# Kernel optimization log

Hardware: AMD Instinct MI355X
Metric: run time of the kernel (lower is better)

## Reference

```python
import jax, jax.numpy as jnp
import numpy as np

NEG_INF = -1e9
EPS = 1e-9


def setup_inputs() -> dict:
    key = jax.random.key(0)
    ks = jax.random.split(key, 8)
    B, N, H = 128, 256, 512
    s = 1.0 / np.sqrt(H)
    u = lambda k, shape: jax.random.uniform(k, shape, jnp.float32, -s, s)
    return {
        "encoder_outputs": jax.random.normal(ks[0], (B, N, H), jnp.float32),
        "w_ih": u(ks[1], (3 * H, H)),
        "w_hh": u(ks[2], (3 * H, H)),
        "b_ih": u(ks[3], (3 * H,)),
        "b_hh": u(ks[4], (3 * H,)),
        "W1": u(ks[5], (H, H)),
        "W2": u(ks[6], (H, H)),
        "v": u(ks[7], (H,)),
        "decode_steps": 32,
    }


def reference(encoder_outputs, w_ih, w_hh, b_ih, b_hh, W1, W2, v, decode_steps):
    B, N, H = encoder_outputs.shape

    # Loop-invariant: W1 @ encoder_outputs (same math as recomputing per step).
    W1e = jnp.einsum('bnh,kh->bnk', encoder_outputs, W1)  # (B, N, H)

    def gru_cell(x, h):
        gi = x @ w_ih.T + b_ih  # (B, 3H)
        gh = h @ w_hh.T + b_hh  # (B, 3H)
        ir, iz, inn = jnp.split(gi, 3, axis=-1)
        hr, hz, hn = jnp.split(gh, 3, axis=-1)
        r = jax.nn.sigmoid(ir + hr)
        z = jax.nn.sigmoid(iz + hz)
        n = jnp.tanh(inn + r * hn)
        return (1.0 - z) * n + z * h

    def step(carry, _):
        h, prev_embed, mask = carry
        h = gru_cell(prev_embed, h)
        W2h = h @ W2.T  # (B, H)
        u = jnp.tanh(W1e + W2h[:, None, :]) @ v  # (B, N)
        u = jnp.where(mask, NEG_INF, u)
        probs = jax.nn.softmax(u, axis=-1)
        idx = jnp.argmax(probs, axis=-1)  # greedy (training=False branch)
        logp = jnp.log(jnp.take_along_axis(probs, idx[:, None], axis=1)[:, 0] + EPS)
        ent = -(probs * jnp.log(probs + EPS)).sum(axis=-1)
        mask = mask | jax.nn.one_hot(idx, N, dtype=bool)
        prev_embed = jnp.take_along_axis(
            encoder_outputs, idx[:, None, None], axis=1)[:, 0, :]
        return (h, prev_embed, mask), (idx, logp, ent)

    h0 = jnp.zeros((B, H), encoder_outputs.dtype)
    prev0 = jnp.zeros((B, H), encoder_outputs.dtype)
    mask0 = jnp.zeros((B, N), dtype=bool)
    _, (idxs, logps, ents) = jax.lax.scan(
        step, (h0, prev0, mask0), None, length=decode_steps)
    # scan stacks on leading (time) axis -> transpose to (B, T) like torch.stack(dim=1)
    return idxs.T, logps.T, ents.T
```

## Files before the change

### kernel.cpp

```cpp
#include <hip/hip_runtime.h>
#include <math.h>

#define BB 128
#define NN 256
#define HH 512
#define T_STEPS 32
#define JQ 128

__device__ __forceinline__ float fast_tanh(float x) {
    float e = __expf(2.0f * x);
    return 1.0f - 2.0f / (1.0f + e);
}
__device__ __forceinline__ float fast_sigmoid(float x) {
    return 1.0f / (1.0f + __expf(-x));
}

#define SW(j, i) ((i) ^ ((((j) >> 2) & 7) << 2))
__global__ __launch_bounds__(256) void w1e_gemm(const float* __restrict__ enc,
                                                const float* __restrict__ W1,
                                                float* __restrict__ W1e) {
    __shared__ float As[32][64];
    __shared__ float Bs[32][64];
    int tid = threadIdx.x;
    int i0 = blockIdx.x * 64;
    int k0 = blockIdx.y * 64;
    int tx = tid & 15, ty = tid >> 4;
    int srow = tid >> 3, sq = tid & 7;

    float acc[4][4];
#pragma unroll
    for (int a = 0; a < 4; a++)
#pragma unroll
        for (int c = 0; c < 4; c++) acc[a][c] = 0.f;

    for (int j0 = 0; j0 < HH; j0 += 32) {
#pragma unroll
        for (int p = 0; p < 2; p++) {
            int row = p * 32 + srow;
            float4 av = *(const float4*)(enc + (size_t)(i0 + row) * HH + j0 + sq * 4);
            float4 bv = *(const float4*)(W1 + (size_t)(k0 + row) * HH + j0 + sq * 4);
#pragma unroll
            for (int c = 0; c < 4; c++) {
                int j = sq * 4 + c;
                float va = (c == 0) ? av.x : (c == 1) ? av.y : (c == 2) ? av.z : av.w;
                float vb = (c == 0) ? bv.x : (c == 1) ? bv.y : (c == 2) ? bv.z : bv.w;
                As[j][SW(j, row)] = va;
                Bs[j][SW(j, row)] = vb;
            }
        }
        __syncthreads();
#pragma unroll
        for (int j = 0; j < 32; j++) {
            float4 a = *(const float4*)&As[j][SW(j, tx * 4)];
            float4 b = *(const float4*)&Bs[j][SW(j, ty * 4)];
            float ar[4] = {a.x, a.y, a.z, a.w};
            float br[4] = {b.x, b.y, b.z, b.w};
#pragma unroll
            for (int ai = 0; ai < 4; ai++)
#pragma unroll
                for (int bk = 0; bk < 4; bk++)
                    acc[ai][bk] += ar[ai] * br[bk];
        }
        __syncthreads();
    }
#pragma unroll
    for (int ai = 0; ai < 4; ai++) {
        float4 r = make_float4(acc[ai][0], acc[ai][1], acc[ai][2], acc[ai][3]);
        *(float4*)(W1e + (size_t)(i0 + tx * 4 + ai) * HH + k0 + ty * 4) = r;
    }
}

__global__ __launch_bounds__(512) void prep_kernel(const float* __restrict__ w_ih,
                                                   const float* __restrict__ w_hh,
                                                   const float* __restrict__ W2,
                                                   float4* __restrict__ gT4,
                                                   float4* __restrict__ w2T4) {
    int bid = blockIdx.x;
    int k = threadIdx.x;
    if (bid < 6 * JQ) {
        int g = bid / JQ, jq = bid % JQ;
        const float* src = (g < 3) ? w_ih : w_hh;
        const float* p = src + (size_t)((g % 3) * HH + k) * HH + jq * 4;
        gT4[(size_t)(g * JQ + jq) * HH + k] = make_float4(p[0], p[1], p[2], p[3]);
    } else {
        int jq = bid - 6 * JQ;
        const float* p = W2 + (size_t)k * HH + jq * 4;
        w2T4[(size_t)jq * HH + k] = make_float4(p[0], p[1], p[2], p[3]);
    }
}

__global__ __launch_bounds__(1024) void decode_kernel(
    const float* __restrict__ enc,
    const float* __restrict__ b_ih, const float* __restrict__ b_hh,
    const float4* __restrict__ gT4, const float4* __restrict__ w2T4,
    const float* __restrict__ v, const float* __restrict__ W1e,
    float* __restrict__ out) {
    __shared__ float x_l[HH];
    __shared__ float h_l[HH];
    __shared__ float vdup[4 * 132];
    __shared__ float w2dup[4 * 132];
    __shared__ float u_l[NN];
    __shared__ int mask_l[NN];
    __shared__ float part[12 * 512];
    __shared__ float wpart[2 * 512];
    __shared__ float redv[16];
    __shared__ int redi[16];
    __shared__ float s_m, s_inv;
    __shared__ int s_idx;

    int b = blockIdx.x, tid = threadIdx.x;
    int k = tid & 511, jh = tid >> 9;
    int jq0 = jh * 64;

    if (tid < HH) { x_l[tid] = 0.f; h_l[tid] = 0.f; }
    if (tid < 512) vdup[(tid >> 7) * 132 + (tid & 127)] = v[tid];
    if (tid < NN) mask_l[tid] = 0;
    __syncthreads();

    for (int t = 0; t < T_STEPS; t++) {
        {
            float a0 = 0.f, a1 = 0.f, a2 = 0.f, a3 = 0.f, a4 = 0.f, a5 = 0.f;
#pragma unroll 2
            for (int jq = jq0; jq < jq0 + 64; jq++) {
                float4 xq = *(const float4*)&x_l[jq * 4];
                float4 hq = *(const float4*)&h_l[jq * 4];
                float4 w0 = gT4[(size_t)(0 * JQ + jq) * HH + k];
                float4 w1 = gT4[(size_t)(1 * JQ + jq) * HH + k];
                float4 w2 = gT4[(size_t)(2 * JQ + jq) * HH + k];
                float4 w3 = gT4[(size_t)(3 * JQ + jq) * HH + k];
                float4 w4 = gT4[(size_t)(4 * JQ + jq) * HH + k];
                float4 w5 = gT4[(size_t)(5 * JQ + jq) * HH + k];
                a0 += xq.x * w0.x + xq.y * w0.y + xq.z * w0.z + xq.w * w0.w;
                a1 += xq.x * w1.x + xq.y * w1.y + xq.z * w1.z + xq.w * w1.w;
                a2 += xq.x * w2.x + xq.y * w2.y + xq.z * w2.z + xq.w * w2.w;
                a3 += hq.x * w3.x + hq.y * w3.y + hq.z * w3.z + hq.w * w3.w;
                a4 += hq.x * w4.x + hq.y * w4.y + hq.z * w4.z + hq.w * w4.w;
                a5 += hq.x * w5.x + hq.y * w5.y + hq.z * w5.z + hq.w * w5.w;
            }
            part[(0 * 2 + jh) * 512 + k] = a0;
            part[(1 * 2 + jh) * 512 + k] = a1;
            part[(2 * 2 + jh) * 512 + k] = a2;
            part[(3 * 2 + jh) * 512 + k] = a3;
            part[(4 * 2 + jh) * 512 + k] = a4;
            part[(5 * 2 + jh) * 512 + k] = a5;
        }
        __syncthreads();
        if (tid < HH) {
            int kk = tid;
            float ir = part[kk] + part[512 + kk];
            float iz = part[1024 + kk] + part[1536 + kk];
            float in = part[2048 + kk] + part[2560 + kk];
            float hr = part[3072 + kk] + part[3584 + kk];
            float hz = part[4096 + kk] + part[4608 + kk];
            float hn = part[5120 + kk] + part[5632 + kk];
            float r = fast_sigmoid(ir + b_ih[kk] + hr + b_hh[kk]);
            float z = fast_sigmoid(iz + b_ih[HH + kk] + hz + b_hh[HH + kk]);
            float n = fast_tanh(in + b_ih[2 * HH + kk] + r * (hn + b_hh[2 * HH + kk]));
            h_l[kk] = (1.f - z) * n + z * h_l[kk];
        }
        __syncthreads();

        {
            float acc = 0.f;
#pragma unroll 4
            for (int jq = jq0; jq < jq0 + 64; jq++) {
                float4 hq = *(const float4*)&h_l[jq * 4];
                float4 w = w2T4[(size_t)jq * HH + k];
                acc += hq.x * w.x + hq.y * w.y + hq.z * w.z + hq.w * w.w;
            }
            wpart[jh * 512 + k] = acc;
        }
        __syncthreads();
        if (tid < 512)
            w2dup[(tid >> 7) * 132 + (tid & 127)] = wpart[tid] + wpart[512 + tid];
        __syncthreads();

        {
            int n = tid >> 2, q = tid & 3;
            const float* Wp = W1e + ((size_t)b * NN + n) * HH + q * 128;
            const float* w2p = w2dup + q * 132;
            const float* vp = vdup + q * 132;
            float p = 0.f;
#pragma unroll 8
            for (int jj = 0; jj < 128; jj += 4) {
                float4 wv = *(const float4*)(Wp + jj);
                float4 av = *(const float4*)(w2p + jj);
                float4 vv = *(const float4*)(vp + jj);
                p += fast_tanh(wv.x + av.x) * vv.x;
                p += fast_tanh(wv.y + av.y) * vv.y;
                p += fast_tanh(wv.z + av.z) * vv.z;
                p += fast_tanh(wv.w + av.w) * vv.w;
            }
            p += __shfl_xor(p, 1);
            p += __shfl_xor(p, 2);
            if (q == 0) u_l[n] = p;
        }
        __syncthreads();

        float val = -3.0e38f;
        if (tid < NN) {
            val = mask_l[tid] ? -1.0e9f : u_l[tid];
            float bv = val;
            int bi = tid;
            int lane = tid & 63;
            for (int off = 32; off > 0; off >>= 1) {
                float ov = __shfl_down(bv, off);
                int oi = __shfl_down(bi, off);
                if (ov > bv || (ov == bv && oi < bi)) { bv = ov; bi = oi; }
            }
            if (lane == 0) { redv[tid >> 6] = bv; redi[tid >> 6] = bi; }
        }
        __syncthreads();
        if (tid == 0) {
            float m = redv[0]; int mi = redi[0];
            for (int w = 1; w < 4; w++)
                if (redv[w] > m || (redv[w] == m && redi[w] < mi)) { m = redv[w]; mi = redi[w]; }
            s_m = m; s_idx = mi;
        }
        __syncthreads();

        if (tid < NN) {
            float d = val - s_m;
            float e = expf(d);
            float ed = e * d;
            int lane = tid & 63;
            for (int off = 32; off > 0; off >>= 1) {
                e += __shfl_down(e, off);
                ed += __shfl_down(ed, off);
            }
            if (lane == 0) { redv[tid >> 6] = e; redv[8 + (tid >> 6)] = ed; }
        }
        __syncthreads();
        if (tid == 0) {
            float S = redv[0] + redv[1] + redv[2] + redv[3];
            float ED = redv[8] + redv[9] + redv[10] + redv[11];
            float inv = 1.0f / S;
            int idx = s_idx;
            out[b * T_STEPS + t] = (float)idx;
            out[BB * T_STEPS + b * T_STEPS + t] = logf(inv + 1e-9f);
            out[2 * BB * T_STEPS + b * T_STEPS + t] = logf(S) - inv * ED;
            mask_l[idx] = 1;
        }
        __syncthreads();
        if (tid < HH) x_l[tid] = enc[((size_t)b * NN + s_idx) * HH + tid];
        __syncthreads();
    }
}

extern "C" void kernel_launch(void* const* d_in, const int* in_sizes, int n_in,
                              void* d_out, int out_size, void* d_ws, size_t ws_size,
                              hipStream_t stream) {
    const float* enc  = (const float*)d_in[0];
    const float* w_ih = (const float*)d_in[1];
    const float* w_hh = (const float*)d_in[2];
    const float* b_ih = (const float*)d_in[3];
    const float* b_hh = (const float*)d_in[4];
    const float* W1   = (const float*)d_in[5];
    const float* W2   = (const float*)d_in[6];
    const float* v    = (const float*)d_in[7];
    float* out = (float*)d_out;

    float* ws = (float*)d_ws;
    float*  W1e  = ws;
    float4* gT4  = (float4*)(W1e + (size_t)BB * NN * HH);
    float4* w2T4 = gT4 + (size_t)6 * JQ * HH;

    w1e_gemm<<<dim3((BB * NN) / 64, HH / 64), 256, 0, stream>>>(enc, W1, W1e);
    prep_kernel<<<7 * JQ, 512, 0, stream>>>(w_ih, w_hh, W2, gT4, w2T4);
    decode_kernel<<<BB, 1024, 0, stream>>>(enc, b_ih, b_hh, gT4, w2T4, v, W1e, out);
}
```

Before: 2.780 ms.

## Process two batch rows per decode block to reuse GRU and W2 weights

The decode kernel now handles two batch rows per 1024-thread block and launches half as many blocks, so each streamed GRU and W2 weight float4 is applied to both rows. This halves weight traffic per row, and weight streaming dominates each step. The attention score loop is also restructured: each wave handles one row and 32 positions, with v and the W2h slice held in registers and a full wave shuffle reduction. Only 64 blocks now run on a device with many more compute units, which lowers parallelism and doubles the per-block W1e streaming.

```diff
diff --git a/kernel.cpp b/kernel.cpp
--- a/kernel.cpp
+++ b/kernel.cpp
@@ -6,6 +6,8 @@
 #define HH 512
 #define T_STEPS 32
 #define JQ 128
+#define RB 2
+#define DBLK (BB/RB)
 
 __device__ __forceinline__ float fast_tanh(float x) {
     float e = __expf(2.0f * x);
@@ -89,160 +91,212 @@
     }
 }
 
+#define PT(r, g, j, kk) part[((((r)*6 + (g)) * 2 + (j)) << 9) + (kk)]
+#define WP(r, j, kk) part[((((r)*2 + (j))) << 9) + (kk)]
+
 __global__ __launch_bounds__(1024) void decode_kernel(
     const float* __restrict__ enc,
     const float* __restrict__ b_ih, const float* __restrict__ b_hh,
     const float4* __restrict__ gT4, const float4* __restrict__ w2T4,
     const float* __restrict__ v, const float* __restrict__ W1e,
     float* __restrict__ out) {
-    __shared__ float x_l[HH];
-    __shared__ float h_l[HH];
-    __shared__ float vdup[4 * 132];
-    __shared__ float w2dup[4 * 132];
-    __shared__ float u_l[NN];
-    __shared__ int mask_l[NN];
-    __shared__ float part[12 * 512];
-    __shared__ float wpart[2 * 512];
-    __shared__ float redv[16];
-    __shared__ int redi[16];
-    __shared__ float s_m, s_inv;
-    __shared__ int s_idx;
-
-    int b = blockIdx.x, tid = threadIdx.x;
+    __shared__ float x_l[RB][HH];
+    __shared__ float h_l[RB][HH];
+    __shared__ float w2l[RB][HH];
+    __shared__ float part[RB * 6 * 2 * 512];
+    __shared__ float ul[RB][NN];
+    __shared__ int mask_l[RB][NN];
+    __shared__ float redm[8];
+    __shared__ int redi[8];
+    __shared__ float redS[8], redE[8];
+    __shared__ float s_m[RB];
+    __shared__ int s_idx[RB];
+
+    int blk = blockIdx.x, tid = threadIdx.x;
+    int sb0 = blk * RB;
+    int lane = tid & 63, wv = tid >> 6;
     int k = tid & 511, jh = tid >> 9;
     int jq0 = jh * 64;
 
-    if (tid < HH) { x_l[tid] = 0.f; h_l[tid] = 0.f; }
-    if (tid < 512) vdup[(tid >> 7) * 132 + (tid & 127)] = v[tid];
-    if (tid < NN) mask_l[tid] = 0;
+    {
+        int r = tid >> 9, j = tid & 511;
+        x_l[r][j] = 0.f;
+        h_l[r][j] = 0.f;
+    }
+    if (tid < 512) mask_l[tid >> 8][tid & 255] = 0;
+
+    float vr[8];
+    {
+        const float* p = v + lane * 8;
+        float4 A = *(const float4*)p;
+        float4 B = *(const float4*)(p + 4);
+        vr[0] = A.x; vr[1] = A.y; vr[2] = A.z; vr[3] = A.w;
+        vr[4] = B.x; vr[5] = B.y; vr[6] = B.z; vr[7] = B.w;
+    }
     __syncthreads();
 
     for (int t = 0; t < T_STEPS; t++) {
         {
-            float a0 = 0.f, a1 = 0.f, a2 = 0.f, a3 = 0.f, a4 = 0.f, a5 = 0.f;
+            float a0 = 0, a1 = 0, a2 = 0, a3 = 0, a4 = 0, a5 = 0;
+            float a6 = 0, a7 = 0, a8 = 0, a9 = 0, a10 = 0, a11 = 0;
 #pragma unroll 2
             for (int jq = jq0; jq < jq0 + 64; jq++) {
-                float4 xq = *(const float4*)&x_l[jq * 4];
-                float4 hq = *(const float4*)&h_l[jq * 4];
+                float4 x0 = *(const float4*)&x_l[0][jq * 4];
+                float4 h0 = *(const float4*)&h_l[0][jq * 4];
+                float4 x1 = *(const float4*)&x_l[1][jq * 4];
+                float4 h1 = *(const float4*)&h_l[1][jq * 4];
                 float4 w0 = gT4[(size_t)(0 * JQ + jq) * HH + k];
                 float4 w1 = gT4[(size_t)(1 * JQ + jq) * HH + k];
                 float4 w2 = gT4[(size_t)(2 * JQ + jq) * HH + k];
                 float4 w3 = gT4[(size_t)(3 * JQ + jq) * HH + k];
                 float4 w4 = gT4[(size_t)(4 * JQ + jq) * HH + k];
                 float4 w5 = gT4[(size_t)(5 * JQ + jq) * HH + k];
-                a0 += xq.x * w0.x + xq.y * w0.y + xq.z * w0.z + xq.w * w0.w;
-                a1 += xq.x * w1.x + xq.y * w1.y + xq.z * w1.z + xq.w * w1.w;
-                a2 += xq.x * w2.x + xq.y * w2.y + xq.z * w2.z + xq.w * w2.w;
-                a3 += hq.x * w3.x + hq.y * w3.y + hq.z * w3.z + hq.w * w3.w;
-                a4 += hq.x * w4.x + hq.y * w4.y + hq.z * w4.z + hq.w * w4.w;
-                a5 += hq.x * w5.x + hq.y * w5.y + hq.z * w5.z + hq.w * w5.w;
-            }
-            part[(0 * 2 + jh) * 512 + k] = a0;
-            part[(1 * 2 + jh) * 512 + k] = a1;
-            part[(2 * 2 + jh) * 512 + k] = a2;
-            part[(3 * 2 + jh) * 512 + k] = a3;
-            part[(4 * 2 + jh) * 512 + k] = a4;
-            part[(5 * 2 + jh) * 512 + k] = a5;
-        }
-        __syncthreads();
-        if (tid < HH) {
-            int kk = tid;
-            float ir = part[kk] + part[512 + kk];
-            float iz = part[1024 + kk] + part[1536 + kk];
-            float in = part[2048 + kk] + part[2560 + kk];
-            float hr = part[3072 + kk] + part[3584 + kk];
-            float hz = part[4096 + kk] + part[4608 + kk];
-            float hn = part[5120 + kk] + part[5632 + kk];
+                a0 += x0.x * w0.x + x0.y * w0.y + x0.z * w0.z + x0.w * w0.w;
+                a1 += x0.x * w1.x + x0.y * w1.y + x0.z * w1.z + x0.w * w1.w;
+                a2 += x0.x * w2.x + x0.y * w2.y + x0.z * w2.z + x0.w * w2.w;
+                a3 += h0.x * w3.x + h0.y * w3.y + h0.z * w3.z + h0.w * w3.w;
+                a4 += h0.x * w4.x + h0.y * w4.y + h0.z * w4.z + h0.w * w4.w;
+                a5 += h0.x * w5.x + h0.y * w5.y + h0.z * w5.z + h0.w * w5.w;
+                a6 += x1.x * w0.x + x1.y * w0.y + x1.z * w0.z + x1.w * w0.w;
+                a7 += x1.x * w1.x + x1.y * w1.y + x1.z * w1.z + x1.w * w1.w;
+                a8 += x1.x * w2.x + x1.y * w2.y + x1.z * w2.z + x1.w * w2.w;
+                a9 += h1.x * w3.x + h1.y * w3.y + h1.z * w3.z + h1.w * w3.w;
+                a10 += h1.x * w4.x + h1.y * w4.y + h1.z * w4.z + h1.w * w4.w;
+                a11 += h1.x * w5.x + h1.y * w5.y + h1.z * w5.z + h1.w * w5.w;
+            }
+            PT(0, 0, jh, k) = a0;  PT(0, 1, jh, k) = a1;  PT(0, 2, jh, k) = a2;
+            PT(0, 3, jh, k) = a3;  PT(0, 4, jh, k) = a4;  PT(0, 5, jh, k) = a5;
+            PT(1, 0, jh, k) = a6;  PT(1, 1, jh, k) = a7;  PT(1, 2, jh, k) = a8;
+            PT(1, 3, jh, k) = a9;  PT(1, 4, jh, k) = a10; PT(1, 5, jh, k) = a11;
+        }
+        __syncthreads();
+        {
+            int rw = tid >> 9, kk = tid & 511;
+            float ir = PT(rw, 0, 0, kk) + PT(rw, 0, 1, kk);
+            float iz = PT(rw, 1, 0, kk) + PT(rw, 1, 1, kk);
+            float inn = PT(rw, 2, 0, kk) + PT(rw, 2, 1, kk);
+            float hr = PT(rw, 3, 0, kk) + PT(rw, 3, 1, kk);
+            float hz = PT(rw, 4, 0, kk) + PT(rw, 4, 1, kk);
+            float hn = PT(rw, 5, 0, kk) + PT(rw, 5, 1, kk);
             float r = fast_sigmoid(ir + b_ih[kk] + hr + b_hh[kk]);
             float z = fast_sigmoid(iz + b_ih[HH + kk] + hz + b_hh[HH + kk]);
-            float n = fast_tanh(in + b_ih[2 * HH + kk] + r * (hn + b_hh[2 * HH + kk]));
-            h_l[kk] = (1.f - z) * n + z * h_l[kk];
-        }
-        __syncthreads();
-
-        {
-            float acc = 0.f;
+            float n = fast_tanh(inn + b_ih[2 * HH + kk] + r * (hn + b_hh[2 * HH + kk]));
+            h_l[rw][kk] = (1.f - z) * n + z * h_l[rw][kk];
+        }
+        __syncthreads();
+
+        {
+            float b0 = 0.f, b1 = 0.f;
 #pragma unroll 4
             for (int jq = jq0; jq < jq0 + 64; jq++) {
-                float4 hq = *(const float4*)&h_l[jq * 4];
+                float4 h0 = *(const float4*)&h_l[0][jq * 4];
+                float4 h1 = *(const float4*)&h_l[1][jq * 4];
                 float4 w = w2T4[(size_t)jq * HH + k];
-                acc += hq.x * w.x + hq.y * w.y + hq.z * w.z + hq.w * w.w;
-            }
-            wpart[jh * 512 + k] = acc;
-        }
-        __syncthreads();
-        if (tid < 512)
-            w2dup[(tid >> 7) * 132 + (tid & 127)] = wpart[tid] + wpart[512 + tid];
-        __syncthreads();
-
-        {
-            int n = tid >> 2, q = tid & 3;
-            const float* Wp = W1e + ((size_t)b * NN + n) * HH + q * 128;
-            const float* w2p = w2dup + q * 132;
-            const float* vp = vdup + q * 132;
-            float p = 0.f;
-#pragma unroll 8
-            for (int jj = 0; jj < 128; jj += 4) {
-                float4 wv = *(const float4*)(Wp + jj);
-                float4 av = *(const float4*)(w2p + jj);
-                float4 vv = *(const float4*)(vp + jj);
-                p += fast_tanh(wv.x + av.x) * vv.x;
-                p += fast_tanh(wv.y + av.y) * vv.y;
-                p += fast_tanh(wv.z + av.z) * vv.z;
-                p += fast_tanh(wv.w + av.w) * vv.w;
-            }
-            p += __shfl_xor(p, 1);
-            p += __shfl_xor(p, 2);
-            if (q == 0) u_l[n] = p;
+                b0 += h0.x * w.x + h0.y * w.y + h0.z * w.z + h0.w * w.w;
+                b1 += h1.x * w.x + h1.y * w.y + h1.z * w.z + h1.w * w.w;
+            }
+            WP(0, jh, k) = b0;
+            WP(1, jh, k) = b1;
+        }
+        __syncthreads();
+        {
+            int rw = tid >> 9, kk = tid & 511;
+            w2l[rw][kk] = WP(rw, 0, kk) + WP(rw, 1, kk);
+        }
+        __syncthreads();
+
+        {
+            int row = wv >> 3, n0 = (wv & 7) * 32;
+            float w2r[8];
+            {
+                const float* p = &w2l[row][lane * 8];
+                float4 A = *(const float4*)p;
+                float4 B = *(const float4*)(p + 4);
+                w2r[0] = A.x; w2r[1] = A.y; w2r[2] = A.z; w2r[3] = A.w;
+                w2r[4] = B.x; w2r[5] = B.y; w2r[6] = B.z; w2r[7] = B.w;
+            }
+            const float* Wb = W1e + (size_t)(sb0 + row) * NN * HH + lane * 8;
+#pragma unroll 4
+            for (int i = 0; i < 32; i++) {
+                int n = n0 + i;
+                const float* Wp = Wb + (size_t)n * HH;
+                float4 A0 = *(const float4*)Wp;
+                float4 A1 = *(const float4*)(Wp + 4);
+                float p = fast_tanh(A0.x + w2r[0]) * vr[0] +
+                          fast_tanh(A0.y + w2r[1]) * vr[1] +
+                          fast_tanh(A0.z + w2r[2]) * vr[2] +
+                          fast_tanh(A0.w + w2r[3]) * vr[3] +
+                          fast_tanh(A1.x + w2r[4]) * vr[4] +
+                          fast_tanh(A1.y + w2r[5]) * vr[5] +
+                          fast_tanh(A1.z + w2r[6]) * vr[6] +
+                          fast_tanh(A1.w + w2r[7]) * vr[7];
+                p += __shfl_xor(p, 1);
+                p += __shfl_xor(p, 2);
+                p += __shfl_xor(p, 4);
+                p += __shfl_xor(p, 8);
+                p += __shfl_xor(p, 16);
+                p += __shfl_xor(p, 32);
+                if (lane == 0) ul[row][n] = p;
+            }
         }
         __syncthreads();
 
         float val = -3.0e38f;
-        if (tid < NN) {
-            val = mask_l[tid] ? -1.0e9f : u_l[tid];
+        int rrow = tid >> 8, nn = tid & 255;
+        if (tid < 512) {
+            val = mask_l[rrow][nn] ? -1.0e9f : ul[rrow][nn];
             float bv = val;
-            int bi = tid;
-            int lane = tid & 63;
+            int bi = nn;
             for (int off = 32; off > 0; off >>= 1) {
                 float ov = __shfl_down(bv, off);
                 int oi = __shfl_down(bi, off);
                 if (ov > bv || (ov == bv && oi < bi)) { bv = ov; bi = oi; }
             }
-            if (lane == 0) { redv[tid >> 6] = bv; redi[tid >> 6] = bi; }
-        }
-        __syncthreads();
-        if (tid == 0) {
-            float m = redv[0]; int mi = redi[0];
-            for (int w = 1; w < 4; w++)
-                if (redv[w] > m || (redv[w] == m && redi[w] < mi)) { m = redv[w]; mi = redi[w]; }
-            s_m = m; s_idx = mi;
-        }
-        __syncthreads();
-
-        if (tid < NN) {
-            float d = val - s_m;
-            float e = expf(d);
+            if (lane == 0) { redm[wv] = bv; redi[wv] = bi; }
+        }
+        __syncthreads();
+        if (tid < 512 && nn == 0) {
+            int base = rrow * 4;
+            float m = redm[base]; int mi = redi[base];
+#pragma unroll
+            for (int w = 1; w < 4; w++) {
+                if (redm[base + w] > m ||
+                    (redm[base + w] == m && redi[base + w] < mi)) {
+                    m = redm[base + w]; mi = redi[base + w];
+                }
+            }
+            s_m[rrow] = m; s_idx[rrow] = mi;
+        }
+        __syncthreads();
+
+        if (tid < 512) {
+            float d = val - s_m[rrow];
+            float e = __expf(d);
             float ed = e * d;
-            int lane = tid & 63;
             for (int off = 32; off > 0; off >>= 1) {
                 e += __shfl_down(e, off);
                 ed += __shfl_down(ed, off);
             }
-            if (lane == 0) { redv[tid >> 6] = e; redv[8 + (tid >> 6)] = ed; }
-        }
-        __syncthreads();
-        if (tid == 0) {
-            float S = redv[0] + redv[1] + redv[2] + redv[3];
-            float ED = redv[8] + redv[9] + redv[10] + redv[11];
+            if (lane == 0) { redS[wv] = e; redE[wv] = ed; }
+        }
+        __syncthreads();
+        if (tid < 512 && nn == 0) {
+            int base = rrow * 4;
+            float S = redS[base] + redS[base + 1] + redS[base + 2] + redS[base + 3];
+            float E = redE[base] + redE[base + 1] + redE[base + 2] + redE[base + 3];
             float inv = 1.0f / S;
-            int idx = s_idx;
-            out[b * T_STEPS + t] = (float)idx;
-            out[BB * T_STEPS + b * T_STEPS + t] = logf(inv + 1e-9f);
-            out[2 * BB * T_STEPS + b * T_STEPS + t] = logf(S) - inv * ED;
-            mask_l[idx] = 1;
-        }
-        __syncthreads();
-        if (tid < HH) x_l[tid] = enc[((size_t)b * NN + s_idx) * HH + tid];
+            int sbr = sb0 + rrow;
+            int idx = s_idx[rrow];
+            out[sbr * T_STEPS + t] = (float)idx;
+            out[BB * T_STEPS + sbr * T_STEPS + t] = logf(inv + 1e-9f);
+            out[2 * BB * T_STEPS + sbr * T_STEPS + t] = logf(S) - inv * E;
+            mask_l[rrow][idx] = 1;
+        }
+        __syncthreads();
+        {
+            int r = tid >> 9, j = tid & 511;
+            x_l[r][j] = enc[((size_t)(sb0 + r) * NN + s_idx[r]) * HH + j];
+        }
         __syncthreads();
     }
 }
@@ -267,5 +321,6 @@
 
     w1e_gemm<<<dim3((BB * NN) / 64, HH / 64), 256, 0, stream>>>(enc, W1, W1e);
     prep_kernel<<<7 * JQ, 512, 0, stream>>>(w_ih, w_hh, W2, gT4, w2T4);
-    decode_kernel<<<BB, 1024, 0, stream>>>(enc, b_ih, b_hh, gT4, w2T4, v, W1e, out);
-}
+    decode_kernel<<<DBLK, 1024, 0, stream>>>(enc, b_ih, b_hh, gT4, w2T4, v,
+                                             W1e, out);
+}
```

Result: slower. 4.001 ms (+43.9%).
